# Performance work log

Measured on AMD Instinct MI355X. Metric: run time of the kernel, lower is better.

The kernel has to match this reference:

```python
import jax, jax.numpy as jnp
import numpy as np

NUM_HEADS = 16
HIDDEN = 1024
DIM = HIDDEN // NUM_HEADS  # 64
NEG = -1e8
LN_EPS = 1e-5


def setup_inputs() -> dict:
    key = jax.random.key(0)
    ks = jax.random.split(key, 8)
    B, Lq, Lk = 8, 512, 2048
    s = 0.02
    return {
        "input_embed": jax.random.normal(ks[0], (B, Lq, HIDDEN), jnp.float32),
        "kg_embed": jax.random.normal(ks[1], (B, Lk, HIDDEN), jnp.float32),
        "input_mask": jnp.ones((B, Lq), jnp.float32),
        "kg_mask": jnp.ones((B, Lk), jnp.float32),
        "Wq": jax.random.normal(ks[2], (DIM, DIM), jnp.float32) * s,
        "Wk": jax.random.normal(ks[3], (DIM, DIM), jnp.float32) * s,
        "Wv": jax.random.normal(ks[4], (DIM, DIM), jnp.float32) * s,
        "W_lin": jax.random.normal(ks[5], (HIDDEN, HIDDEN), jnp.float32) * s,
        "b_lin": jnp.zeros((HIDDEN,), jnp.float32),
        "ln_gamma": jnp.ones((HIDDEN,), jnp.float32),
        "ln_beta": jnp.zeros((HIDDEN,), jnp.float32),
    }


def reference(input_embed, kg_embed, input_mask, kg_mask, Wq, Wk, Wv, W_lin, b_lin, ln_gamma, ln_beta):
    B, Lq, H = input_embed.shape
    Lk = kg_embed.shape[1]
    # split heads: per-head slices share the SAME dim x dim q/k/v weights
    xq = input_embed.reshape(B, Lq, NUM_HEADS, DIM)
    xk = kg_embed.reshape(B, Lk, NUM_HEADS, DIM)
    q = jnp.einsum('bqhd,ed->bqhe', xq, Wq)  # Linear: x @ W.T
    k = jnp.einsum('bkhd,ed->bkhe', xk, Wk)
    v = jnp.einsum('bkhd,ed->bkhe', xk, Wv)
    scores = jnp.einsum('bqhd,bkhd->bhqk', q, k) / np.sqrt(DIM)  # [B,H,Lq,Lk]
    # additive masks: query-side and key-side
    scores = scores + ((1.0 - input_mask) * NEG)[:, None, :, None] \
                    + ((1.0 - kg_mask) * NEG)[:, None, None, :]
    attn = jax.nn.softmax(scores, axis=-1)
    ctx = jnp.einsum('bhqk,bkhd->bqhd', attn, v).reshape(B, Lq, H)  # concat heads
    lin = ctx @ W_lin.T + b_lin
    x = jax.nn.gelu(lin, approximate=False) + input_embed  # nn.GELU() is exact erf
    mu = jnp.mean(x, axis=-1, keepdims=True)
    var = jnp.mean(jnp.square(x - mu), axis=-1, keepdims=True)
    return (x - mu) * jax.lax.rsqrt(var + LN_EPS) * ln_gamma + ln_beta
```

## Files before the change

kernel.cpp:

```cpp
#include <hip/hip_runtime.h>
#include <cstdint>

#define BATCH 8
#define LQ 512
#define LK 2048
#define NH 16
#define DIM 64
#define HID 1024
#define NTOK (BATCH * LQ)
#define NKT (LK / 64)
#define SC 0.1803368801111204f
#define NEGM (-1.4426950408889634e8f)

typedef _Float16 f16x8 __attribute__((ext_vector_type(8)));
typedef __fp16 half2v __attribute__((ext_vector_type(2)));
typedef float f32x4 __attribute__((ext_vector_type(4)));

#define MFMA(a, b, c) __builtin_amdgcn_mfma_f32_16x16x32_f16((a), (b), (c), 0, 0, 0)

__device__ __forceinline__ f16x8 ld8(const _Float16* p) { return *(const f16x8*)p; }

__device__ __forceinline__ void gl_lds16(const void* g, void* l) {
  __builtin_amdgcn_global_load_lds(
      (const __attribute__((address_space(1))) uint32_t*)g,
      (__attribute__((address_space(3))) uint32_t*)l, 16, 0, 0);
}

__device__ __forceinline__ f16x8 cvt8(const float* p) {
  const float4 a = *(const float4*)p;
  const float4 b = *(const float4*)(p + 4);
  f16x8 v;
  v[0] = (_Float16)a.x; v[1] = (_Float16)a.y; v[2] = (_Float16)a.z; v[3] = (_Float16)a.w;
  v[4] = (_Float16)b.x; v[5] = (_Float16)b.y; v[6] = (_Float16)b.z; v[7] = (_Float16)b.w;
  return v;
}

__device__ __forceinline__ uint2 pk4(float a, float b, float c, float d) {
  union { half2v h2[2]; uint2 u; } t;
  t.h2[0] = __builtin_amdgcn_cvt_pkrtz(a, b);
  t.h2[1] = __builtin_amdgcn_cvt_pkrtz(c, d);
  return t.u;
}

__device__ __forceinline__ f16x8 pk8(float4 a, float4 b) {
  union { half2v h2[4]; f16x8 v; } t;
  t.h2[0] = __builtin_amdgcn_cvt_pkrtz(a.x, a.y);
  t.h2[1] = __builtin_amdgcn_cvt_pkrtz(a.z, a.w);
  t.h2[2] = __builtin_amdgcn_cvt_pkrtz(b.x, b.y);
  t.h2[3] = __builtin_amdgcn_cvt_pkrtz(b.z, b.w);
  return t.v;
}

__global__ __launch_bounds__(512, 2) void attn_kernel(
    const float* __restrict__ Xq, const float* __restrict__ Xk,
    const float* __restrict__ Wq, const float* __restrict__ Wk,
    const float* __restrict__ Wv, const float* __restrict__ kg_mask,
    _Float16* __restrict__ ctx) {
  __shared__ __align__(16) float    Xl[2][64 * 64];
  __shared__ __align__(16) _Float16 Kl[64 * 72];
  __shared__ __align__(16) _Float16 Vl[64 * 72];
  __shared__ __align__(16) _Float16 Pl[8][2][16 * 72];
  __shared__ __align__(16) float    Ml[LK];
  const int tid = threadIdx.x;
  const int wave = tid >> 6, lane = tid & 63, l16 = lane & 15, quad = lane >> 4;
  const int kw = wave & 3;
  const int b = blockIdx.x >> 4, h = blockIdx.x & 15;
  const int qbase = blockIdx.y * 256;
  const float* Xg = Xk + (size_t)b * LK * HID + h * 64;
  const float* mg = kg_mask + (size_t)b * LK;

  auto stageX = [&](int kt, int nbuf) {
#pragma unroll
    for (int i = 0; i < 2; ++i) {
      const int row = i * 32 + wave * 4 + (lane >> 4);
      const int c = (lane & 15) ^ (row & 7);
      gl_lds16(Xg + (size_t)(kt + row) * HID + c * 4,
               &Xl[nbuf][(i * 32 + wave * 4) * 64]);
    }
  };
  stageX(0, 0);

  {
    const float4 m4 = *(const float4*)(mg + tid * 4);
    float4 mo;
    mo.x = (1.f - m4.x) * NEGM;
    mo.y = (1.f - m4.y) * NEGM;
    mo.z = (1.f - m4.z) * NEGM;
    mo.w = (1.f - m4.w) * NEGM;
    *(float4*)(Ml + tid * 4) = mo;
  }

  f16x8 aq0[2], aq1[2];
  {
    f16x8 wq0[4], wq1[4];
#pragma unroll
    for (int nt = 0; nt < 4; ++nt) {
      const float* wp = Wq + (nt * 16 + l16) * DIM + quad * 8;
      wq0[nt] = cvt8(wp);
      wq1[nt] = cvt8(wp + 32);
    }
#pragma unroll
    for (int qt = 0; qt < 2; ++qt) {
      const int qg = qbase + wave * 32 + qt * 16 + l16;
      const float* xpq = Xq + (size_t)(b * LQ + qg) * HID + h * 64 + quad * 8;
      const f16x8 bq0 = cvt8(xpq), bq1 = cvt8(xpq + 32);
#pragma unroll
      for (int nt = 0; nt < 4; ++nt) {
        f32x4 d = {0.f, 0.f, 0.f, 0.f};
        d = MFMA(wq0[nt], bq0, d);
        d = MFMA(wq1[nt], bq1, d);
        *(uint2*)&Pl[wave][qt][l16 * 72 + nt * 16 + quad * 4] =
            pk4(d[0] * SC, d[1] * SC, d[2] * SC, d[3] * SC);
      }
      aq0[qt] = ld8(&Pl[wave][qt][l16 * 72 + quad * 8]);
      aq1[qt] = ld8(&Pl[wave][qt][l16 * 72 + 32 + quad * 8]);
    }
  }

  const float* Wsel = (wave < 4) ? Wk : Wv;
  f16x8 aw0[4], aw1[4];
#pragma unroll
  for (int nt = 0; nt < 4; ++nt) {
    const float* wp = Wsel + (nt * 16 + l16) * DIM + quad * 8;
    aw0[nt] = cvt8(wp);
    aw1[nt] = cvt8(wp + 32);
  }

  const f32x4 z4 = {0.f, 0.f, 0.f, 0.f};
  f32x4 o[2][4];
  float l_run[2] = {0.f, 0.f};
#pragma unroll
  for (int qt = 0; qt < 2; ++qt)
#pragma unroll
    for (int i = 0; i < 4; ++i) o[qt][i] = z4;

  for (int t = 0; t < NKT; ++t) {
    const int buf = t & 1;
    const int kt = t * 64;
    __syncthreads();

    const int rr = kw * 16 + l16;
    const float* xrow = &Xl[buf][rr * 64];
    const int sw8 = l16 & 7;
    const float4 c0 = *(const float4*)(xrow + (((2 * quad) ^ sw8) * 4));
    const float4 c1 = *(const float4*)(xrow + (((2 * quad + 1) ^ sw8) * 4));
    const float4 c2 = *(const float4*)(xrow + (((2 * quad + 8) ^ sw8) * 4));
    const float4 c3 = *(const float4*)(xrow + (((2 * quad + 9) ^ sw8) * 4));
    const f16x8 bx0 = pk8(c0, c1), bx1 = pk8(c2, c3);

    if (wave < 4) {
#pragma unroll
      for (int nt = 0; nt < 4; ++nt) {
        f32x4 d = z4;
        d = MFMA(aw0[nt], bx0, d);
        d = MFMA(aw1[nt], bx1, d);
        *(uint2*)&Kl[rr * 72 + nt * 16 + quad * 4] =
            pk4(d[0], d[1], d[2], d[3]);
      }
    } else {
#pragma unroll
      for (int dt = 0; dt < 4; ++dt) {
        f32x4 d = z4;
        d = MFMA(bx0, aw0[dt], d);
        d = MFMA(bx1, aw1[dt], d);
        *(uint2*)&Vl[(dt * 16 + l16) * 72 + kw * 16 + quad * 4] =
            pk4(d[0], d[1], d[2], d[3]);
      }
    }
    __syncthreads();

    if (t + 1 < NKT) stageX(kt + 64, buf ^ 1);

    float4 mv[4];
#pragma unroll
    for (int nt = 0; nt < 4; ++nt)
      mv[nt] = *(const float4*)(Ml + kt + nt * 16 + quad * 4);

    float p[2][4][4];
#pragma unroll
    for (int nt = 0; nt < 4; ++nt) {
      const f16x8 kb0 = ld8(&Kl[(nt * 16 + l16) * 72 + quad * 8]);
      const f16x8 kb1 = ld8(&Kl[(nt * 16 + l16) * 72 + 32 + quad * 8]);
#pragma unroll
      for (int qt = 0; qt < 2; ++qt) {
        f32x4 s = z4;
        s = MFMA(kb0, aq0[qt], s);
        s = MFMA(kb1, aq1[qt], s);
        const float e0 = __builtin_amdgcn_exp2f(s[0] + mv[nt].x);
        const float e1 = __builtin_amdgcn_exp2f(s[1] + mv[nt].y);
        const float e2 = __builtin_amdgcn_exp2f(s[2] + mv[nt].z);
        const float e3 = __builtin_amdgcn_exp2f(s[3] + mv[nt].w);
        l_run[qt] += (e0 + e1) + (e2 + e3);
        p[qt][nt][0] = e0; p[qt][nt][1] = e1; p[qt][nt][2] = e2; p[qt][nt][3] = e3;
      }
    }
#pragma unroll
    for (int qt = 0; qt < 2; ++qt)
#pragma unroll
      for (int nt = 0; nt < 4; ++nt)
        *(uint2*)&Pl[wave][qt][l16 * 72 + nt * 16 + quad * 4] =
            pk4(p[qt][nt][0], p[qt][nt][1], p[qt][nt][2], p[qt][nt][3]);
    f16x8 ap0[2], ap1[2];
#pragma unroll
    for (int qt = 0; qt < 2; ++qt) {
      ap0[qt] = ld8(&Pl[wave][qt][l16 * 72 + quad * 8]);
      ap1[qt] = ld8(&Pl[wave][qt][l16 * 72 + 32 + quad * 8]);
    }
#pragma unroll
    for (int dt = 0; dt < 4; ++dt) {
      const f16x8 vb0 = ld8(&Vl[(dt * 16 + l16) * 72 + quad * 8]);
      const f16x8 vb1 = ld8(&Vl[(dt * 16 + l16) * 72 + 32 + quad * 8]);
#pragma unroll
      for (int qt = 0; qt < 2; ++qt) {
        o[qt][dt] = MFMA(vb0, ap0[qt], o[qt][dt]);
        o[qt][dt] = MFMA(vb1, ap1[qt], o[qt][dt]);
      }
    }
  }

  float inv[2];
#pragma unroll
  for (int qt = 0; qt < 2; ++qt) {
    float s = l_run[qt];
    s += __shfl_xor(s, 16);
    s += __shfl_xor(s, 32);
    inv[qt] = 1.f / s;
  }
#pragma unroll
  for (int qt = 0; qt < 2; ++qt) {
    const int qg = qbase + wave * 32 + qt * 16 + l16;
    _Float16* base = ctx + (size_t)(b * LQ + qg) * HID + h * 64;
#pragma unroll
    for (int dt = 0; dt < 4; ++dt)
      *(uint2*)(base + dt * 16 + quad * 4) =
          pk4(o[qt][dt][0] * inv[qt], o[qt][dt][1] * inv[qt],
              o[qt][dt][2] * inv[qt], o[qt][dt][3] * inv[qt]);
  }
}

__global__ __launch_bounds__(256) void wconv_kernel(const float* __restrict__ W,
                                                    _Float16* __restrict__ Wh) {
  const int i = blockIdx.x * 256 + threadIdx.x;
  const float4 v = ((const float4*)W)[i];
  ((uint2*)Wh)[i] = pk4(v.x, v.y, v.z, v.w);
}

__global__ __launch_bounds__(512) void linear_kernel(const _Float16* __restrict__ A,
                                                     const _Float16* __restrict__ Wh,
                                                     const float* __restrict__ bias,
                                                     const float* __restrict__ resid,
                                                     float* __restrict__ Xout) {
  __shared__ __align__(16) _Float16 Al[2][128 * 64];
  __shared__ __align__(16) _Float16 Bl[2][128 * 64];
  const int tid = threadIdx.x;
  const int wave = tid >> 6, lane = tid & 63, l16 = lane & 15, quad = lane >> 4;
  const int wm = wave >> 2, wn = wave & 3;
  const int nbase = blockIdx.x * 128, mbase = blockIdx.y * 128;
  const int srow = wave * 16 + (lane >> 3);
  const int sc = lane & 7;

  auto stage = [&](int kk, int nbuf) {
#pragma unroll
    for (int i = 0; i < 2; ++i) {
      const int row = srow + i * 8;
      const int c = sc ^ (row & 7);
      gl_lds16(A + (size_t)(mbase + row) * HID + kk + c * 8,
               &Al[nbuf][(wave * 16 + i * 8) * 64]);
      gl_lds16(Wh + (size_t)(nbase + row) * HID + kk + c * 8,
               &Bl[nbuf][(wave * 16 + i * 8) * 64]);
    }
  };

  const f32x4 z4 = {0.f, 0.f, 0.f, 0.f};
  f32x4 acc[4][2];
#pragma unroll
  for (int mt = 0; mt < 4; ++mt)
#pragma unroll
    for (int nt = 0; nt < 2; ++nt) acc[mt][nt] = z4;

  stage(0, 0);
  for (int t = 0; t < HID / 64; ++t) {
    const int buf = t & 1;
    __syncthreads();
    if (t + 1 < HID / 64) stage((t + 1) * 64, buf ^ 1);
    const int sw = l16 & 7;
    f16x8 b0[2], b1[2];
#pragma unroll
    for (int nt = 0; nt < 2; ++nt) {
      const int brow = wn * 32 + nt * 16 + l16;
      b0[nt] = ld8(&Bl[buf][brow * 64 + (quad ^ sw) * 8]);
      b1[nt] = ld8(&Bl[buf][brow * 64 + ((quad + 4) ^ sw) * 8]);
    }
#pragma unroll
    for (int mt = 0; mt < 4; ++mt) {
      const int arow = wm * 64 + mt * 16 + l16;
      const f16x8 a0 = ld8(&Al[buf][arow * 64 + (quad ^ sw) * 8]);
      const f16x8 a1 = ld8(&Al[buf][arow * 64 + ((quad + 4) ^ sw) * 8]);
#pragma unroll
      for (int nt = 0; nt < 2; ++nt) {
        acc[mt][nt] = MFMA(a0, b0[nt], acc[mt][nt]);
        acc[mt][nt] = MFMA(a1, b1[nt], acc[mt][nt]);
      }
    }
  }
#pragma unroll
  for (int nt = 0; nt < 2; ++nt) {
    const int col = nbase + wn * 32 + nt * 16 + l16;
    const float bv = bias[col];
#pragma unroll
    for (int mt = 0; mt < 4; ++mt) {
#pragma unroll
      for (int r = 0; r < 4; ++r) {
        const int row = mbase + wm * 64 + mt * 16 + quad * 4 + r;
        const float v = acc[mt][nt][r] + bv;
        const float g = 0.5f * v * (1.f + erff(v * 0.70710678118654752f));
        Xout[(size_t)row * HID + col] = g + resid[(size_t)row * HID + col];
      }
    }
  }
}

__global__ __launch_bounds__(256) void ln_kernel(const float* __restrict__ X,
                                                 const float* __restrict__ gamma,
                                                 const float* __restrict__ beta,
                                                 float* __restrict__ out) {
  const int row = blockIdx.x, tid = threadIdx.x;
  const int lane = tid & 63, wave = tid >> 6;
  const float4 v = *(const float4*)(X + (size_t)row * HID + tid * 4);
  float s1 = v.x + v.y + v.z + v.w;
  float s2 = v.x * v.x + v.y * v.y + v.z * v.z + v.w * v.w;
#pragma unroll
  for (int off = 1; off < 64; off <<= 1) {
    s1 += __shfl_xor(s1, off);
    s2 += __shfl_xor(s2, off);
  }
  __shared__ float r1[4], r2[4];
  if (lane == 0) { r1[wave] = s1; r2[wave] = s2; }
  __syncthreads();
  s1 = r1[0] + r1[1] + r1[2] + r1[3];
  s2 = r2[0] + r2[1] + r2[2] + r2[3];
  const float mu = s1 * (1.f / HID);
  const float var = s2 * (1.f / HID) - mu * mu;
  const float rstd = rsqrtf(var + 1e-5f);
  const float4 g = *(const float4*)(gamma + tid * 4);
  const float4 be = *(const float4*)(beta + tid * 4);
  float4 ov;
  ov.x = (v.x - mu) * rstd * g.x + be.x;
  ov.y = (v.y - mu) * rstd * g.y + be.y;
  ov.z = (v.z - mu) * rstd * g.z + be.z;
  ov.w = (v.w - mu) * rstd * g.w + be.w;
  *(float4*)(out + (size_t)row * HID + tid * 4) = ov;
}

extern "C" void kernel_launch(void* const* d_in, const int* in_sizes, int n_in,
                              void* d_out, int out_size, void* d_ws, size_t ws_size,
                              hipStream_t stream) {
  (void)in_sizes; (void)n_in; (void)out_size; (void)ws_size;
  const float* input_embed = (const float*)d_in[0];
  const float* kg_embed    = (const float*)d_in[1];
  const float* kg_mask = (const float*)d_in[3];
  const float* Wq    = (const float*)d_in[4];
  const float* Wk    = (const float*)d_in[5];
  const float* Wv    = (const float*)d_in[6];
  const float* W_lin = (const float*)d_in[7];
  const float* b_lin = (const float*)d_in[8];
  const float* gamma = (const float*)d_in[9];
  const float* beta  = (const float*)d_in[10];

  char* ws = (char*)d_ws;
  _Float16* ctx = (_Float16*)(ws);
  float*    Xb  = (float*)(ws + (8u << 20));
  _Float16* Wh  = (_Float16*)(ws + (24u << 20));

  attn_kernel<<<dim3(128, 2), dim3(512), 0, stream>>>(input_embed, kg_embed, Wq, Wk, Wv,
                                                      kg_mask, ctx);
  wconv_kernel<<<dim3(1024), dim3(256), 0, stream>>>(W_lin, Wh);
  linear_kernel<<<dim3(8, 32), dim3(512), 0, stream>>>(ctx, Wh, b_lin, input_embed, Xb);
  ln_kernel<<<dim3(NTOK), dim3(256), 0, stream>>>(Xb, gamma, beta, (float*)d_out);
}
```

Before: 216.6 us.

## Software-pipeline K/V projection with register prefetch and double-buffered K/V LDS

Replaces the LDS staging of raw fp32 kg_embed tiles with direct per-thread global loads into registers, prefetched two tiles ahead. K/V for the next tile are projected into a second LDS buffer while the current tile's attention runs, so each iteration needs one barrier instead of two. It also raises wave priority around the MFMA sections. In exchange it uses more registers and doubles the K/V LDS footprint while removing the fp32 X buffers. Global load latency is now exposed in registers rather than hidden by async LDS copies.

```diff
diff --git a/kernel.cpp b/kernel.cpp
--- a/kernel.cpp
+++ b/kernel.cpp
@@ -26,6 +26,11 @@
       (__attribute__((address_space(3))) uint32_t*)l, 16, 0, 0);
 }
 
+__device__ __forceinline__ void lds_barrier() {
+  asm volatile("s_waitcnt lgkmcnt(0)" ::: "memory");
+  __builtin_amdgcn_s_barrier();
+}
+
 __device__ __forceinline__ f16x8 cvt8(const float* p) {
   const float4 a = *(const float4*)p;
   const float4 b = *(const float4*)(p + 4);
@@ -56,9 +61,8 @@
     const float* __restrict__ Wq, const float* __restrict__ Wk,
     const float* __restrict__ Wv, const float* __restrict__ kg_mask,
     _Float16* __restrict__ ctx) {
-  __shared__ __align__(16) float    Xl[2][64 * 64];
-  __shared__ __align__(16) _Float16 Kl[64 * 72];
-  __shared__ __align__(16) _Float16 Vl[64 * 72];
+  __shared__ __align__(16) _Float16 Kl[2][64 * 72];
+  __shared__ __align__(16) _Float16 Vl[2][64 * 72];
   __shared__ __align__(16) _Float16 Pl[8][2][16 * 72];
   __shared__ __align__(16) float    Ml[LK];
   const int tid = threadIdx.x;
@@ -69,16 +73,16 @@
   const float* Xg = Xk + (size_t)b * LK * HID + h * 64;
   const float* mg = kg_mask + (size_t)b * LK;
 
-  auto stageX = [&](int kt, int nbuf) {
-#pragma unroll
-    for (int i = 0; i < 2; ++i) {
-      const int row = i * 32 + wave * 4 + (lane >> 4);
-      const int c = (lane & 15) ^ (row & 7);
-      gl_lds16(Xg + (size_t)(kt + row) * HID + c * 4,
-               &Xl[nbuf][(i * 32 + wave * 4) * 64]);
-    }
+  const float* xrow0 = Xg + (size_t)(kw * 16 + l16) * HID + quad * 8;
+  float4 xf0, xf1, xf2, xf3;
+  auto loadX = [&](int kt) {
+    const float* xr = xrow0 + (size_t)kt * HID;
+    xf0 = *(const float4*)(xr);
+    xf1 = *(const float4*)(xr + 4);
+    xf2 = *(const float4*)(xr + 32);
+    xf3 = *(const float4*)(xr + 36);
   };
-  stageX(0, 0);
+  loadX(0);
 
   {
     const float4 m4 = *(const float4*)(mg + tid * 4);
@@ -127,34 +131,16 @@
   }
 
   const f32x4 z4 = {0.f, 0.f, 0.f, 0.f};
-  f32x4 o[2][4];
-  float l_run[2] = {0.f, 0.f};
-#pragma unroll
-  for (int qt = 0; qt < 2; ++qt)
-#pragma unroll
-    for (int i = 0; i < 4; ++i) o[qt][i] = z4;
-
-  for (int t = 0; t < NKT; ++t) {
-    const int buf = t & 1;
-    const int kt = t * 64;
-    __syncthreads();
-
-    const int rr = kw * 16 + l16;
-    const float* xrow = &Xl[buf][rr * 64];
-    const int sw8 = l16 & 7;
-    const float4 c0 = *(const float4*)(xrow + (((2 * quad) ^ sw8) * 4));
-    const float4 c1 = *(const float4*)(xrow + (((2 * quad + 1) ^ sw8) * 4));
-    const float4 c2 = *(const float4*)(xrow + (((2 * quad + 8) ^ sw8) * 4));
-    const float4 c3 = *(const float4*)(xrow + (((2 * quad + 9) ^ sw8) * 4));
-    const f16x8 bx0 = pk8(c0, c1), bx1 = pk8(c2, c3);
-
+
+  {
+    const f16x8 bx0 = pk8(xf0, xf1), bx1 = pk8(xf2, xf3);
     if (wave < 4) {
 #pragma unroll
       for (int nt = 0; nt < 4; ++nt) {
         f32x4 d = z4;
         d = MFMA(aw0[nt], bx0, d);
         d = MFMA(aw1[nt], bx1, d);
-        *(uint2*)&Kl[rr * 72 + nt * 16 + quad * 4] =
+        *(uint2*)&Kl[0][(kw * 16 + l16) * 72 + nt * 16 + quad * 4] =
             pk4(d[0], d[1], d[2], d[3]);
       }
     } else {
@@ -163,13 +149,48 @@
         f32x4 d = z4;
         d = MFMA(bx0, aw0[dt], d);
         d = MFMA(bx1, aw1[dt], d);
-        *(uint2*)&Vl[(dt * 16 + l16) * 72 + kw * 16 + quad * 4] =
+        *(uint2*)&Vl[0][(dt * 16 + l16) * 72 + kw * 16 + quad * 4] =
             pk4(d[0], d[1], d[2], d[3]);
       }
     }
-    __syncthreads();
-
-    if (t + 1 < NKT) stageX(kt + 64, buf ^ 1);
+  }
+  loadX(64);
+  lds_barrier();
+
+  f32x4 o[2][4];
+  float l_run[2] = {0.f, 0.f};
+#pragma unroll
+  for (int qt = 0; qt < 2; ++qt)
+#pragma unroll
+    for (int i = 0; i < 4; ++i) o[qt][i] = z4;
+
+  for (int t = 0; t < NKT; ++t) {
+    const int buf = t & 1;
+    const int kt = t * 64;
+
+    if (t + 1 < NKT) {
+      const f16x8 bx0 = pk8(xf0, xf1), bx1 = pk8(xf2, xf3);
+      if (wave < 4) {
+#pragma unroll
+        for (int nt = 0; nt < 4; ++nt) {
+          f32x4 d = z4;
+          d = MFMA(aw0[nt], bx0, d);
+          d = MFMA(aw1[nt], bx1, d);
+          *(uint2*)&Kl[buf ^ 1][(kw * 16 + l16) * 72 + nt * 16 + quad * 4] =
+              pk4(d[0], d[1], d[2], d[3]);
+        }
+      } else {
+#pragma unroll
+        for (int dt = 0; dt < 4; ++dt) {
+          f32x4 d = z4;
+          d = MFMA(bx0, aw0[dt], d);
+          d = MFMA(bx1, aw1[dt], d);
+          *(uint2*)&Vl[buf ^ 1][(dt * 16 + l16) * 72 + kw * 16 + quad * 4] =
+              pk4(d[0], d[1], d[2], d[3]);
+        }
+      }
+      if (t + 2 < NKT) loadX(kt + 128);
+    }
 
     float4 mv[4];
 #pragma unroll
@@ -177,10 +198,11 @@
       mv[nt] = *(const float4*)(Ml + kt + nt * 16 + quad * 4);
 
     float p[2][4][4];
+    __builtin_amdgcn_s_setprio(1);
 #pragma unroll
     for (int nt = 0; nt < 4; ++nt) {
-      const f16x8 kb0 = ld8(&Kl[(nt * 16 + l16) * 72 + quad * 8]);
-      const f16x8 kb1 = ld8(&Kl[(nt * 16 + l16) * 72 + 32 + quad * 8]);
+      const f16x8 kb0 = ld8(&Kl[buf][(nt * 16 + l16) * 72 + quad * 8]);
+      const f16x8 kb1 = ld8(&Kl[buf][(nt * 16 + l16) * 72 + 32 + quad * 8]);
 #pragma unroll
       for (int qt = 0; qt < 2; ++qt) {
         f32x4 s = z4;
@@ -194,6 +216,8 @@
         p[qt][nt][0] = e0; p[qt][nt][1] = e1; p[qt][nt][2] = e2; p[qt][nt][3] = e3;
       }
     }
+    __builtin_amdgcn_s_setprio(0);
+
 #pragma unroll
     for (int qt = 0; qt < 2; ++qt)
 #pragma unroll
@@ -206,16 +230,21 @@
       ap0[qt] = ld8(&Pl[wave][qt][l16 * 72 + quad * 8]);
       ap1[qt] = ld8(&Pl[wave][qt][l16 * 72 + 32 + quad * 8]);
     }
+
+    __builtin_amdgcn_s_setprio(1);
 #pragma unroll
     for (int dt = 0; dt < 4; ++dt) {
-      const f16x8 vb0 = ld8(&Vl[(dt * 16 + l16) * 72 + quad * 8]);
-      const f16x8 vb1 = ld8(&Vl[(dt * 16 + l16) * 72 + 32 + quad * 8]);
+      const f16x8 vb0 = ld8(&Vl[buf][(dt * 16 + l16) * 72 + quad * 8]);
+      const f16x8 vb1 = ld8(&Vl[buf][(dt * 16 + l16) * 72 + 32 + quad * 8]);
 #pragma unroll
       for (int qt = 0; qt < 2; ++qt) {
         o[qt][dt] = MFMA(vb0, ap0[qt], o[qt][dt]);
         o[qt][dt] = MFMA(vb1, ap1[qt], o[qt][dt]);
       }
     }
+    __builtin_amdgcn_s_setprio(0);
+
+    lds_barrier();
   }
 
   float inv[2];
```

Result: no change. 213.8 us (-1.3%).
